# Performance work log

Hardware: AMD Instinct MI355X
Metric: run time of the kernel (lower is better)

## Reference

```python
import math
import jax, jax.numpy as jnp
import numpy as np

BS, N, NH_N, NH_E, NH_Y, H = 2, 256, 256, 128, 128, 8
F = NH_N // H  # per-head feature dim


def _lin(x, w, b):
    # w stored as (in, out): out = x @ w + b
    return x @ w + b


def setup_inputs() -> dict:
    key = jax.random.key(0)
    ks = iter(jax.random.split(key, 64))
    def w(shape, s=0.02):
        return jax.random.normal(next(ks), shape, dtype=jnp.float32) * s
    inp = {
        'x': jax.random.normal(next(ks), (BS, N, NH_N), dtype=jnp.float32),
        'a': jax.random.normal(next(ks), (BS, N, N, NH_E), dtype=jnp.float32),
        'y': jax.random.normal(next(ks), (BS, NH_Y), dtype=jnp.float32),
        'qw': w((NH_N, NH_N)), 'qb': w((NH_N,)),
        'kw': w((NH_N, NH_N)), 'kb': w((NH_N,)),
        'vw': w((NH_N, NH_N)), 'vb': w((NH_N,)),
        'a2x_add_w': w((NH_E, NH_N)), 'a2x_add_b': w((NH_N,)),
        'a2x_mul_w': w((NH_E, NH_N)), 'a2x_mul_b': w((NH_N,)),
        'y2e_mul_w': w((NH_Y, NH_N)), 'y2e_mul_b': w((NH_N,)),
        'y2e_add_w': w((NH_Y, NH_N)), 'y2e_add_b': w((NH_N,)),
        'y2x_mul_w': w((NH_Y, NH_N)), 'y2x_mul_b': w((NH_N,)),
        'y2x_add_w': w((NH_Y, NH_N)), 'y2x_add_b': w((NH_N,)),
        'y_y_w': w((NH_Y, NH_Y)), 'y_y_b': w((NH_Y,)),
        'x_y_w': w((4 * NH_N, NH_Y)), 'x_y_b': w((NH_Y,)),
        'a_y_w': w((4 * NH_E, NH_Y)), 'a_y_b': w((NH_Y,)),
        'x_out_w': w((NH_N, NH_N)), 'x_out_b': w((NH_N,)),
        'a_out_w': w((NH_N, NH_E)), 'a_out_b': w((NH_E,)),
        'y_out1_w': w((NH_Y, NH_Y)), 'y_out1_b': w((NH_Y,)),
        'y_out2_w': w((NH_Y, NH_Y)), 'y_out2_b': w((NH_Y,)),
    }
    return inp


def reference(x, a, y, qw, qb, kw, kb, vw, vb,
              a2x_add_w, a2x_add_b, a2x_mul_w, a2x_mul_b,
              y2e_mul_w, y2e_mul_b, y2e_add_w, y2e_add_b,
              y2x_mul_w, y2x_mul_b, y2x_add_w, y2x_add_b,
              y_y_w, y_y_b, x_y_w, x_y_b, a_y_w, a_y_b,
              x_out_w, x_out_b, a_out_w, a_out_b,
              y_out1_w, y_out1_b, y_out2_w, y_out2_b):
    bs, n, _ = x.shape
    Q = _lin(x, qw, qb).reshape(bs, n, H, F)
    K = _lin(x, kw, kb).reshape(bs, n, H, F)
    # Feature-wise outer product (never reduced over F): (bs, n, n, H, F)
    Y = (Q[:, :, None] * K[:, None, :]) / math.sqrt(F)
    a1 = _lin(a, a2x_add_w, a2x_add_b).reshape(bs, n, n, H, F)
    a2 = _lin(a, a2x_mul_w, a2x_mul_b).reshape(bs, n, n, H, F)
    Y = Y * (a1 + 1.0) + a2
    # edge output path
    ahat = Y.reshape(bs, n, n, NH_N)
    ye1 = _lin(y, y2e_add_w, y2e_add_b)[:, None, None]
    ye2 = _lin(y, y2e_mul_w, y2e_mul_b)[:, None, None]
    ahat = _lin(ye1 + (ye2 + 1.0) * ahat, a_out_w, a_out_b)
    # node output path: softmax over the second node axis (dim=2)
    attn = jax.nn.softmax(Y, axis=2)
    V = _lin(x, vw, vb).reshape(bs, n, H, F)
    wV = jnp.einsum('bijhf,bjhf->bihf', attn, V).reshape(bs, n, NH_N)
    yx1 = _lin(y, y2x_add_w, y2x_add_b)[:, None]
    yx2 = _lin(y, y2x_mul_w, y2x_mul_b)[:, None]
    xhat = _lin(yx1 + (yx2 + 1.0) * wV, x_out_w, x_out_b)
    # global output path (Xtoy / Atoy use unbiased std, ddof=1 as in torch.std)
    zx = jnp.concatenate([x.mean(axis=1), x.min(axis=1), x.max(axis=1),
                          jnp.std(x, axis=1, ddof=1)], axis=-1)
    za = jnp.concatenate([a.mean(axis=(1, 2)), a.min(axis=(1, 2)), a.max(axis=(1, 2)),
                          jnp.std(a, axis=(1, 2), ddof=1)], axis=-1)
    yhat = _lin(y, y_y_w, y_y_b) + _lin(za, a_y_w, a_y_b) + _lin(zx, x_y_w, x_y_b)
    yhat = _lin(jax.nn.relu(_lin(yhat, y_out1_w, y_out1_b)), y_out2_w, y_out2_b)
    return (xhat, ahat, yhat)
```

## Files before the change

kernel.cpp:

```cpp
#include <hip/hip_runtime.h>
#include <hip/hip_bf16.h>
#include <cstddef>

constexpr int BS = 2;
constexpr int N  = 256;
constexpr int D  = 256;
constexpr int E  = 128;
constexpr int YD = 128;
constexpr float RSQRT_F = 0.17677669529663687f;

typedef __attribute__((ext_vector_type(8))) short     short8;
typedef __attribute__((ext_vector_type(4))) float     f32x4;
typedef __attribute__((ext_vector_type(4))) unsigned short u16x4;
typedef __attribute__((ext_vector_type(8))) unsigned short u16x8;

__device__ __forceinline__ unsigned short f2bf(float x) {
    unsigned u = __float_as_uint(x);
    unsigned r = (u + 0x7fffu + ((u >> 16) & 1u)) >> 16;
    return (unsigned short)r;
}
__device__ __forceinline__ float bf2f(unsigned short h) {
    return __uint_as_float(((unsigned)h) << 16);
}
__device__ __forceinline__ f32x4 mfma16(short8 a, short8 b, f32x4 c) {
    return __builtin_amdgcn_mfma_f32_16x16x32_bf16(a, b, c, 0, 0, 0);
}

__global__ __launch_bounds__(256) void prep_kernel(
        const float* __restrict__ x, const float* __restrict__ a,
        const float* __restrict__ y,
        const float* __restrict__ qw, const float* __restrict__ qb,
        const float* __restrict__ kw, const float* __restrict__ kb,
        const float* __restrict__ vw, const float* __restrict__ vb,
        const float* __restrict__ Wadd, const float* __restrict__ Wmul,
        const float* __restrict__ W2,
        const float* __restrict__ we_add, const float* __restrict__ be_add,
        const float* __restrict__ we_mul, const float* __restrict__ be_mul,
        const float* __restrict__ wx_add, const float* __restrict__ bx_add,
        const float* __restrict__ wx_mul, const float* __restrict__ bx_mul,
        float* __restrict__ Q, unsigned short* __restrict__ kvJ,
        unsigned short* __restrict__ WaddT, unsigned short* __restrict__ WmulT,
        unsigned short* __restrict__ W2T,
        float* __restrict__ ye1, float* __restrict__ ye2,
        float* __restrict__ yx1, float* __restrict__ yx2,
        float* __restrict__ psum, float* __restrict__ psumsq,
        float* __restrict__ pmin, float* __restrict__ pmax,
        float* __restrict__ zx) {
    const int blk = blockIdx.x;
    const int tid = threadIdx.x;
    __shared__ float smem[4096];

    if (blk < 192) {
        const int m  = blk >> 6;
        const int rg = blk & 63;
        const float* W = (m == 0) ? qw : (m == 1) ? kw : vw;
        const float* B = (m == 0) ? qb : (m == 1) ? kb : vb;
        float (*xs)[D] = (float(*)[D])smem;
#pragma unroll
        for (int r = 0; r < 8; ++r)
            xs[r][tid] = x[(size_t)(rg * 8 + r) * D + tid];
        __syncthreads();
        float acc[8];
        const float bb = B[tid];
#pragma unroll
        for (int r = 0; r < 8; ++r) acc[r] = bb;
#pragma unroll 4
        for (int k = 0; k < D; ++k) {
            const float w = W[k * D + tid];
#pragma unroll
            for (int r = 0; r < 8; ++r) acc[r] += xs[r][k] * w;
        }
#pragma unroll
        for (int r = 0; r < 8; ++r) {
            const int row = rg * 8 + r;
            if (m == 0) Q[(size_t)row * D + tid] = acc[r];
            else        kvJ[((size_t)row * D + tid) * 2 + (m - 1)] = f2bf(acc[r]);
        }
    } else if (blk < 576) {
        int idx = (blk - 192) * 256 + tid;
        int s = idx >> 15;
        int k = idx & 32767;
        if (s == 0)      { int f = k >> 7, e = k & 127; WaddT[k] = f2bf(Wadd[e * 256 + f]); }
        else if (s == 1) { int f = k >> 7, e = k & 127; WmulT[k] = f2bf(Wmul[e * 256 + f]); }
        else             { int f = k & 255, e = k >> 8; W2T[k]   = f2bf(W2[f * 128 + e]); }
    } else if (blk < 584) {
        const int bb = (blk - 576) >> 2;
        const int m  = (blk - 576) & 3;
        const float* W; const float* B; float* O;
        switch (m) {
            case 0:  W = we_add; B = be_add; O = ye1; break;
            case 1:  W = we_mul; B = be_mul; O = ye2; break;
            case 2:  W = wx_add; B = bx_add; O = yx1; break;
            default: W = wx_mul; B = bx_mul; O = yx2; break;
        }
        float acc = B[tid];
#pragma unroll 4
        for (int k = 0; k < YD; ++k)
            acc += y[bb * YD + k] * W[k * D + tid];
        O[bb * D + tid] = acc;
    } else if (blk < 600) {
        const int bb = (blk - 584) >> 3;
        const int fc = (blk - 584) & 7;
        const int fl = tid & 31;
        const int ig = tid >> 5;
        const int f  = fc * 32 + fl;
        float s = 0.f, ss = 0.f, mn = INFINITY, mx = -INFINITY;
#pragma unroll 4
        for (int i = ig * 32; i < ig * 32 + 32; ++i) {
            const float v = x[((size_t)bb * N + i) * D + f];
            s += v; ss += v * v; mn = fminf(mn, v); mx = fmaxf(mx, v);
        }
        smem[0 * 256 + ig * 32 + fl] = s;
        smem[1 * 256 + ig * 32 + fl] = ss;
        smem[2 * 256 + ig * 32 + fl] = mn;
        smem[3 * 256 + ig * 32 + fl] = mx;
        __syncthreads();
        if (ig == 0) {
#pragma unroll
            for (int gg = 1; gg < 8; ++gg) {
                s += smem[0 * 256 + gg * 32 + fl]; ss += smem[1 * 256 + gg * 32 + fl];
                mn = fminf(mn, smem[2 * 256 + gg * 32 + fl]);
                mx = fmaxf(mx, smem[3 * 256 + gg * 32 + fl]);
            }
            const float M = 256.f;
            const float mean = s / M;
            const float var  = (ss - s * s / M) / (M - 1.f);
            zx[bb * 1024 + f]       = mean;
            zx[bb * 1024 + 256 + f] = mn;
            zx[bb * 1024 + 512 + f] = mx;
            zx[bb * 1024 + 768 + f] = sqrtf(fmaxf(var, 0.f));
        }
    } else {
        const int bi2 = blk - 600;
        const int te  = tid & 31;
        const int tj  = tid >> 5;
        const float* base = a + (size_t)bi2 * N * E + te * 4;
        f32x4 s4  = (f32x4){0.f, 0.f, 0.f, 0.f};
        f32x4 ss4 = (f32x4){0.f, 0.f, 0.f, 0.f};
        f32x4 mn4 = (f32x4){INFINITY, INFINITY, INFINITY, INFINITY};
        f32x4 mx4 = (f32x4){-INFINITY, -INFINITY, -INFINITY, -INFINITY};
#pragma unroll 4
        for (int j = tj * 32; j < tj * 32 + 32; ++j) {
            const f32x4 v = *(const f32x4*)(base + (size_t)j * E);
            s4 += v;
            ss4.x = fmaf(v.x, v.x, ss4.x); ss4.y = fmaf(v.y, v.y, ss4.y);
            ss4.z = fmaf(v.z, v.z, ss4.z); ss4.w = fmaf(v.w, v.w, ss4.w);
            mn4.x = fminf(mn4.x, v.x); mn4.y = fminf(mn4.y, v.y);
            mn4.z = fminf(mn4.z, v.z); mn4.w = fminf(mn4.w, v.w);
            mx4.x = fmaxf(mx4.x, v.x); mx4.y = fmaxf(mx4.y, v.y);
            mx4.z = fmaxf(mx4.z, v.z); mx4.w = fmaxf(mx4.w, v.w);
        }
        *(f32x4*)(smem + (0 * 8 + tj) * 128 + te * 4) = s4;
        *(f32x4*)(smem + (1 * 8 + tj) * 128 + te * 4) = ss4;
        *(f32x4*)(smem + (2 * 8 + tj) * 128 + te * 4) = mn4;
        *(f32x4*)(smem + (3 * 8 + tj) * 128 + te * 4) = mx4;
        __syncthreads();
        if (tid < 128) {
            float s = 0.f, ss = 0.f, mn = INFINITY, mx = -INFINITY;
#pragma unroll
            for (int g = 0; g < 8; ++g) {
                s  += smem[(0 * 8 + g) * 128 + tid];
                ss += smem[(1 * 8 + g) * 128 + tid];
                mn = fminf(mn, smem[(2 * 8 + g) * 128 + tid]);
                mx = fmaxf(mx, smem[(3 * 8 + g) * 128 + tid]);
            }
            const int o = bi2 * E + tid;
            psum[o] = s; psumsq[o] = ss; pmin[o] = mn; pmax[o] = mx;
        }
    }
}

__global__ __launch_bounds__(512, 1) void main_kernel(
        const float* __restrict__ a,
        const unsigned short* __restrict__ WaddT, const float* __restrict__ Badd,
        const unsigned short* __restrict__ WmulT, const float* __restrict__ Bmul,
        const unsigned short* __restrict__ W2T,  const float* __restrict__ AoutB,
        const float* __restrict__ Q, const unsigned short* __restrict__ kvJ,
        const float* __restrict__ ye1, const float* __restrict__ ye2,
        float* __restrict__ ahat, float* __restrict__ wV) {
    const int bi = ((blockIdx.x & 7) << 6) | (blockIdx.x >> 3);
    const int b  = bi >> 8;
    const int tid  = threadIdx.x;
    const int lane = tid & 63;
    const int w    = tid >> 6;
    const int l15  = lane & 15;
    const int lk   = lane >> 4;

    __shared__ unsigned short abuf[2][32 * 128];
    __shared__ unsigned short hbuf[2][32 * 256];

    const float* arow = a + (size_t)bi * (N * E);
    float* ahatp      = ahat + (size_t)bi * (N * E);
    const unsigned short* kvb = kvJ + (size_t)b * N * D * 2;

    short8 waf[4][2], wmf[4][2], w2f[8];
#pragma unroll
    for (int ks = 0; ks < 4; ++ks)
#pragma unroll
        for (int m_ = 0; m_ < 2; ++m_) {
            const int frow = w * 32 + m_ * 16 + l15;
            waf[ks][m_] = *(const short8*)(WaddT + frow * 128 + ks * 32 + lk * 8);
            wmf[ks][m_] = *(const short8*)(WmulT + frow * 128 + ks * 32 + lk * 8);
        }
#pragma unroll
    for (int ks = 0; ks < 8; ++ks)
        w2f[ks] = *(const short8*)(W2T + (w * 16 + l15) * 256 + ks * 32 + lk * 8);

    float qs[8], e1c[8], e2c[8], b1c[8], b2c[8];
#pragma unroll
    for (int m_ = 0; m_ < 2; ++m_) {
        const int f0 = w * 32 + m_ * 16 + lk * 4;
        const f32x4 qv = *(const f32x4*)(Q + (size_t)bi * D + f0);
        const f32x4 a1 = *(const f32x4*)(ye1 + b * D + f0);
        const f32x4 a2 = *(const f32x4*)(ye2 + b * D + f0);
        const f32x4 bb1 = *(const f32x4*)(Badd + f0);
        const f32x4 bb2 = *(const f32x4*)(Bmul + f0);
#pragma unroll
        for (int r = 0; r < 4; ++r) {
            const int fi = m_ * 4 + r;
            qs[fi]  = qv[r] * RSQRT_F;
            e1c[fi] = a1[r];
            e2c[fi] = a2[r] + 1.f;
            b1c[fi] = bb1[r] + 1.f;
            b2c[fi] = bb2[r];
        }
    }
    const f32x4 bias2 = *(const f32x4*)(AoutB + w * 16 + lk * 4);

    float sm_l[8], sm_a[8];
#pragma unroll
    for (int q = 0; q < 8; ++q) { sm_l[q] = 0.f; sm_a[q] = 0.f; }

    const int sjl = tid >> 4;
    const int seq = tid & 15;
    const unsigned saddr = ((unsigned)(sjl * 256 + seq * 16)) ^ ((unsigned)(sjl & 7) << 4);

    {
        const float* ap = arow + (size_t)sjl * E + seq * 8;
        const f32x4 v0 = *(const f32x4*)ap;
        const f32x4 v1 = *(const f32x4*)(ap + 4);
        u16x8 pk;
        pk.s0 = f2bf(v0.x); pk.s1 = f2bf(v0.y); pk.s2 = f2bf(v0.z); pk.s3 = f2bf(v0.w);
        pk.s4 = f2bf(v1.x); pk.s5 = f2bf(v1.y); pk.s6 = f2bf(v1.z); pk.s7 = f2bf(v1.w);
        *(u16x8*)((char*)abuf[0] + saddr) = pk;
    }
    __syncthreads();

    for (int t = 0; t < 8; ++t) {
        const int j0 = t * 32;
        const unsigned short* ab = abuf[t & 1];
        unsigned short* hw = hbuf[t & 1];

        f32x4 p0, p1;
        if (t < 7) {
            const float* ap = arow + (size_t)(j0 + 32 + sjl) * E + seq * 8;
            p0 = *(const f32x4*)ap;
            p1 = *(const f32x4*)(ap + 4);
        }
        u16x8 kvv[2][2];
#pragma unroll
        for (int n_ = 0; n_ < 2; ++n_) {
            const int jg = j0 + n_ * 16 + l15;
#pragma unroll
            for (int m_ = 0; m_ < 2; ++m_)
                kvv[n_][m_] = *(const u16x8*)(kvb + ((size_t)jg * D + w * 32 + m_ * 16 + lk * 4) * 2);
        }

        f32x4 acc1[2][2], acc2[2][2];
#pragma unroll
        for (int m_ = 0; m_ < 2; ++m_) {
            const f32x4 i1 = (f32x4){b1c[m_ * 4 + 0], b1c[m_ * 4 + 1], b1c[m_ * 4 + 2], b1c[m_ * 4 + 3]};
            const f32x4 i2 = (f32x4){b2c[m_ * 4 + 0], b2c[m_ * 4 + 1], b2c[m_ * 4 + 2], b2c[m_ * 4 + 3]};
#pragma unroll
            for (int n_ = 0; n_ < 2; ++n_) { acc1[m_][n_] = i1; acc2[m_][n_] = i2; }
        }
#pragma unroll
        for (int ks = 0; ks < 4; ++ks) {
            short8 bfrg[2];
#pragma unroll
            for (int n_ = 0; n_ < 2; ++n_) {
                const int jrow = n_ * 16 + l15;
                const unsigned baddr = ((unsigned)(jrow * 256 + (ks * 32 + lk * 8) * 2))
                                       ^ ((unsigned)(jrow & 7) << 4);
                bfrg[n_] = *(const short8*)((const char*)ab + baddr);
            }
#pragma unroll
            for (int m_ = 0; m_ < 2; ++m_)
#pragma unroll
                for (int n_ = 0; n_ < 2; ++n_) {
                    acc1[m_][n_] = mfma16(waf[ks][m_], bfrg[n_], acc1[m_][n_]);
                    acc2[m_][n_] = mfma16(wmf[ks][m_], bfrg[n_], acc2[m_][n_]);
                }
        }

#pragma unroll
        for (int n_ = 0; n_ < 2; ++n_) {
            const int jrow = n_ * 16 + l15;
#pragma unroll
            for (int m_ = 0; m_ < 2; ++m_) {
                u16x4 hp;
#pragma unroll
                for (int r = 0; r < 4; ++r) {
                    const int fi = m_ * 4 + r;
                    const float kf = bf2f(kvv[n_][m_][2 * r]);
                    const float vf = bf2f(kvv[n_][m_][2 * r + 1]);
                    const float yv = qs[fi] * kf * acc1[m_][n_][r] + acc2[m_][n_][r];
                    hp[r] = f2bf(e1c[fi] + e2c[fi] * yv);
                    const float ev = __expf(yv);
                    sm_l[fi] += ev;
                    sm_a[fi] += ev * vf;
                }
                const unsigned haddr = ((unsigned)(jrow * 512 + (w * 32 + m_ * 16 + lk * 4) * 2))
                                       ^ ((unsigned)(jrow & 7) << 4);
                *(u16x4*)((char*)hw + haddr) = hp;
            }
        }

        if (t < 7) {
            u16x8 pk;
            pk.s0 = f2bf(p0.x); pk.s1 = f2bf(p0.y); pk.s2 = f2bf(p0.z); pk.s3 = f2bf(p0.w);
            pk.s4 = f2bf(p1.x); pk.s5 = f2bf(p1.y); pk.s6 = f2bf(p1.z); pk.s7 = f2bf(p1.w);
            *(u16x8*)((char*)abuf[(t + 1) & 1] + saddr) = pk;
        }
        __syncthreads();

        f32x4 accO[2];
        accO[0] = bias2; accO[1] = bias2;
#pragma unroll
        for (int ks = 0; ks < 8; ++ks) {
            const int foff = ks * 32 + lk * 8;
#pragma unroll
            for (int n2 = 0; n2 < 2; ++n2) {
                const int jrow = n2 * 16 + l15;
                const unsigned haddr = ((unsigned)(jrow * 512 + foff * 2))
                                       ^ ((unsigned)(jrow & 7) << 4);
                const short8 hf = *(const short8*)((const char*)hw + haddr);
                accO[n2] = mfma16(w2f[ks], hf, accO[n2]);
            }
        }
        {
            const int eb = w * 16 + lk * 4;
#pragma unroll
            for (int n2 = 0; n2 < 2; ++n2) {
                const int jg2 = j0 + n2 * 16 + l15;
                *(f32x4*)(ahatp + (size_t)jg2 * E + eb) = accO[n2];
            }
        }
    }

#pragma unroll
    for (int st = 1; st <= 8; st <<= 1) {
#pragma unroll
        for (int fi = 0; fi < 8; ++fi) {
            sm_l[fi] += __shfl_xor(sm_l[fi], st, 64);
            sm_a[fi] += __shfl_xor(sm_a[fi], st, 64);
        }
    }
    if (l15 == 0) {
#pragma unroll
        for (int m_ = 0; m_ < 2; ++m_)
#pragma unroll
            for (int r = 0; r < 4; ++r) {
                const int fi = m_ * 4 + r;
                const int f  = w * 32 + m_ * 16 + lk * 4 + r;
                wV[(size_t)bi * D + f] = sm_a[fi] / sm_l[fi];
            }
    }
}

__global__ __launch_bounds__(256) void post_kernel(
        const float* __restrict__ wV,
        const float* __restrict__ yx1, const float* __restrict__ yx2,
        const float* __restrict__ W, const float* __restrict__ B,
        const float* __restrict__ psum, const float* __restrict__ psumsq,
        const float* __restrict__ pmin, const float* __restrict__ pmax,
        float* __restrict__ xhat, float* __restrict__ za) {
    const int blk = blockIdx.x;
    const int tid = threadIdx.x;
    __shared__ float smem[2048];

    if (blk < 64) {
        float (*xr)[D] = (float(*)[D])smem;
#pragma unroll
        for (int r = 0; r < 8; ++r) {
            const int row = blk * 8 + r;
            const int b = row >> 8;
            xr[r][tid] = yx1[b * D + tid] + (yx2[b * D + tid] + 1.f) * wV[(size_t)row * D + tid];
        }
        __syncthreads();
        float acc[8];
        const float bb = B[tid];
#pragma unroll
        for (int r = 0; r < 8; ++r) acc[r] = bb;
#pragma unroll 4
        for (int k = 0; k < D; ++k) {
            const float w = W[k * D + tid];
#pragma unroll
            for (int r = 0; r < 8; ++r) acc[r] += xr[r][k] * w;
        }
#pragma unroll
        for (int r = 0; r < 8; ++r)
            xhat[(size_t)(blk * 8 + r) * D + tid] = acc[r];
    } else {
        const int b = blk - 64;
        const int feat = tid & 127;
        const int g = tid >> 7;
        float s = 0.f, ss = 0.f, mn = INFINITY, mx = -INFINITY;
#pragma unroll 4
        for (int c = g * 128; c < g * 128 + 128; ++c) {
            const int o = (b * 256 + c) * E + feat;
            s += psum[o]; ss += psumsq[o];
            mn = fminf(mn, pmin[o]); mx = fmaxf(mx, pmax[o]);
        }
        smem[0 * 256 + g * 128 + feat] = s;
        smem[1 * 256 + g * 128 + feat] = ss;
        smem[2 * 256 + g * 128 + feat] = mn;
        smem[3 * 256 + g * 128 + feat] = mx;
        __syncthreads();
        if (g == 0) {
            s += smem[0 * 256 + 128 + feat]; ss += smem[1 * 256 + 128 + feat];
            mn = fminf(mn, smem[2 * 256 + 128 + feat]);
            mx = fmaxf(mx, smem[3 * 256 + 128 + feat]);
            const float M = 65536.f;
            const float mean = s / M;
            const float var  = (ss - s * s / M) / (M - 1.f);
            za[b * 512 + feat]       = mean;
            za[b * 512 + 128 + feat] = mn;
            za[b * 512 + 256 + feat] = mx;
            za[b * 512 + 384 + feat] = sqrtf(fmaxf(var, 0.f));
        }
    }
}

__global__ __launch_bounds__(128) void yhat_partial_kernel(
        const float* __restrict__ y,
        const float* __restrict__ za, const float* __restrict__ zx,
        const float* __restrict__ yyw, const float* __restrict__ ayw,
        const float* __restrict__ xyw,
        float* __restrict__ partial) {
    const int b = blockIdx.x >> 6 ? 1 : 0;
    const int bb = blockIdx.x / 52;
    const int c  = blockIdx.x - bb * 52;
    const int o  = threadIdx.x;
    const int k0 = c * 32;
    float p = 0.f;
    if (k0 < 128) {
#pragma unroll 8
        for (int k = k0; k < k0 + 32; ++k) p += y[bb * YD + k] * yyw[k * YD + o];
    } else if (k0 < 640) {
        const int kk = k0 - 128;
#pragma unroll 8
        for (int k = kk; k < kk + 32; ++k) p += za[bb * 512 + k] * ayw[k * YD + o];
    } else {
        const int kk = k0 - 640;
#pragma unroll 8
        for (int k = kk; k < kk + 32; ++k) p += zx[bb * 1024 + k] * xyw[k * YD + o];
    }
    (void)b;
    partial[(bb * 52 + c) * YD + o] = p;
}

__global__ __launch_bounds__(512) void yhat_finish_kernel(
        const float* __restrict__ partial,
        const float* __restrict__ yyb, const float* __restrict__ xyb,
        const float* __restrict__ ayb,
        const float* __restrict__ w1, const float* __restrict__ b1,
        const float* __restrict__ w2, const float* __restrict__ b2,
        float* __restrict__ out) {
    const int b = blockIdx.x;
    const int tid = threadIdx.x;
    const int o = tid & 127;
    const int q = tid >> 7;
    __shared__ float red[4][128];
    __shared__ float h1s[128], h2s[128];
    float s = 0.f;
#pragma unroll 13
    for (int c = q * 13; c < q * 13 + 13; ++c)
        s += partial[(b * 52 + c) * YD + o];
    red[q][o] = s;
    __syncthreads();
    if (tid < 128)
        h1s[o] = yyb[o] + xyb[o] + ayb[o] + red[0][o] + red[1][o] + red[2][o] + red[3][o];
    __syncthreads();
    float p2 = 0.f;
#pragma unroll 8
    for (int k = q * 32; k < q * 32 + 32; ++k) p2 += h1s[k] * w1[k * YD + o];
    red[q][o] = p2;
    __syncthreads();
    if (tid < 128) h2s[o] = fmaxf(b1[o] + red[0][o] + red[1][o] + red[2][o] + red[3][o], 0.f);
    __syncthreads();
    float p3 = 0.f;
#pragma unroll 8
    for (int k = q * 32; k < q * 32 + 32; ++k) p3 += h2s[k] * w2[k * YD + o];
    red[q][o] = p3;
    __syncthreads();
    if (tid < 128) out[b * YD + o] = b2[o] + red[0][o] + red[1][o] + red[2][o] + red[3][o];
}

extern "C" void kernel_launch(void* const* d_in, const int* in_sizes, int n_in,
                              void* d_out, int out_size, void* d_ws, size_t ws_size,
                              hipStream_t stream) {
    const float* x         = (const float*)d_in[0];
    const float* a         = (const float*)d_in[1];
    const float* y         = (const float*)d_in[2];
    const float* qw        = (const float*)d_in[3];  const float* qb        = (const float*)d_in[4];
    const float* kw        = (const float*)d_in[5];  const float* kb        = (const float*)d_in[6];
    const float* vw        = (const float*)d_in[7];  const float* vb        = (const float*)d_in[8];
    const float* a2x_add_w = (const float*)d_in[9];  const float* a2x_add_b = (const float*)d_in[10];
    const float* a2x_mul_w = (const float*)d_in[11]; const float* a2x_mul_b = (const float*)d_in[12];
    const float* y2e_mul_w = (const float*)d_in[13]; const float* y2e_mul_b = (const float*)d_in[14];
    const float* y2e_add_w = (const float*)d_in[15]; const float* y2e_add_b = (const float*)d_in[16];
    const float* y2x_mul_w = (const float*)d_in[17]; const float* y2x_mul_b = (const float*)d_in[18];
    const float* y2x_add_w = (const float*)d_in[19]; const float* y2x_add_b = (const float*)d_in[20];
    const float* y_y_w     = (const float*)d_in[21]; const float* y_y_b     = (const float*)d_in[22];
    const float* x_y_w     = (const float*)d_in[23]; const float* x_y_b     = (const float*)d_in[24];
    const float* a_y_w     = (const float*)d_in[25]; const float* a_y_b     = (const float*)d_in[26];
    const float* x_out_w   = (const float*)d_in[27]; const float* x_out_b   = (const float*)d_in[28];
    const float* a_out_w   = (const float*)d_in[29]; const float* a_out_b   = (const float*)d_in[30];
    const float* y_out1_w  = (const float*)d_in[31]; const float* y_out1_b  = (const float*)d_in[32];
    const float* y_out2_w  = (const float*)d_in[33]; const float* y_out2_b  = (const float*)d_in[34];

    float* ws = (float*)d_ws;
    float* Q      = ws;
    unsigned short* kvJ = (unsigned short*)(ws + 131072);
    float* wV     = ws + 262144;
    float* ye1    = ws + 393216;
    float* ye2    = ws + 393728;
    float* yx1    = ws + 394240;
    float* yx2    = ws + 394752;
    float* psum   = ws + 395264;
    float* psumsq = ws + 460800;
    float* pminb  = ws + 526336;
    float* pmaxb  = ws + 591872;
    float* za     = ws + 657408;
    float* zx     = ws + 658432;
    unsigned short* WaddT = (unsigned short*)(ws + 660480);
    unsigned short* WmulT = (unsigned short*)(ws + 676864);
    unsigned short* W2T   = (unsigned short*)(ws + 693248);
    float* ypart  = ws + 709632;

    float* xhat = (float*)d_out;
    float* ahat = (float*)d_out + 131072;
    float* yhat = (float*)d_out + 16908288;

    prep_kernel<<<1112, 256, 0, stream>>>(
        x, a, y, qw, qb, kw, kb, vw, vb,
        a2x_add_w, a2x_mul_w, a_out_w,
        y2e_add_w, y2e_add_b, y2e_mul_w, y2e_mul_b,
        y2x_add_w, y2x_add_b, y2x_mul_w, y2x_mul_b,
        Q, kvJ, WaddT, WmulT, W2T,
        ye1, ye2, yx1, yx2,
        psum, psumsq, pminb, pmaxb, zx);
    main_kernel<<<512, 512, 0, stream>>>(a, WaddT, a2x_add_b, WmulT, a2x_mul_b,
                                         W2T, a_out_b, Q, kvJ, ye1, ye2, ahat, wV);
    post_kernel<<<66, 256, 0, stream>>>(wV, yx1, yx2, x_out_w, x_out_b,
                                        psum, psumsq, pminb, pmaxb, xhat, za);
    yhat_partial_kernel<<<104, 128, 0, stream>>>(y, za, zx, y_y_w, a_y_w, x_y_w, ypart);
    yhat_finish_kernel<<<2, 512, 0, stream>>>(ypart, y_y_b, x_y_b, a_y_b,
                                              y_out1_w, y_out1_b, y_out2_w, y_out2_b, yhat);
}
```

Before: 115.8 us.

## Double j-tile to 64 rows per iteration in main kernel, halving barriers

The main kernel now processes 64 edge rows per pipeline step instead of 32, with doubled LDS buffers. That halves the loop iterations and __syncthreads count and issues four prefetch loads per thread with a new staging layout. It also switches bf16 conversion to the HIP intrinsic, raises one unroll factor, and drops the occupancy hint from launch bounds. The cost is doubled shared memory (about 96KB) and more live registers, which may limit occupancy or cause spills.

```diff
diff --git a/kernel.cpp b/kernel.cpp
--- a/kernel.cpp
+++ b/kernel.cpp
@@ -1,6 +1,7 @@
 #include <hip/hip_runtime.h>
 #include <hip/hip_bf16.h>
 #include <cstddef>
+#include <cstring>
 
 constexpr int BS = 2;
 constexpr int N  = 256;
@@ -15,9 +16,10 @@
 typedef __attribute__((ext_vector_type(8))) unsigned short u16x8;
 
 __device__ __forceinline__ unsigned short f2bf(float x) {
-    unsigned u = __float_as_uint(x);
-    unsigned r = (u + 0x7fffu + ((u >> 16) & 1u)) >> 16;
-    return (unsigned short)r;
+    __hip_bfloat16 h = __float2bfloat16(x);
+    unsigned short r;
+    __builtin_memcpy(&r, &h, 2);
+    return r;
 }
 __device__ __forceinline__ float bf2f(unsigned short h) {
     return __uint_as_float(((unsigned)h) << 16);
@@ -139,7 +141,7 @@
         f32x4 ss4 = (f32x4){0.f, 0.f, 0.f, 0.f};
         f32x4 mn4 = (f32x4){INFINITY, INFINITY, INFINITY, INFINITY};
         f32x4 mx4 = (f32x4){-INFINITY, -INFINITY, -INFINITY, -INFINITY};
-#pragma unroll 4
+#pragma unroll 8
         for (int j = tj * 32; j < tj * 32 + 32; ++j) {
             const f32x4 v = *(const f32x4*)(base + (size_t)j * E);
             s4 += v;
@@ -170,7 +172,7 @@
     }
 }
 
-__global__ __launch_bounds__(512, 1) void main_kernel(
+__global__ __launch_bounds__(512) void main_kernel(
         const float* __restrict__ a,
         const unsigned short* __restrict__ WaddT, const float* __restrict__ Badd,
         const unsigned short* __restrict__ WmulT, const float* __restrict__ Bmul,
@@ -186,8 +188,8 @@
     const int l15  = lane & 15;
     const int lk   = lane >> 4;
 
-    __shared__ unsigned short abuf[2][32 * 128];
-    __shared__ unsigned short hbuf[2][32 * 256];
+    __shared__ unsigned short abuf[2][64 * 128];
+    __shared__ unsigned short hbuf[2][64 * 256];
 
     const float* arow = a + (size_t)bi * (N * E);
     float* ahatp      = ahat + (size_t)bi * (N * E);
@@ -210,9 +212,9 @@
 #pragma unroll
     for (int m_ = 0; m_ < 2; ++m_) {
         const int f0 = w * 32 + m_ * 16 + lk * 4;
-        const f32x4 qv = *(const f32x4*)(Q + (size_t)bi * D + f0);
-        const f32x4 a1 = *(const f32x4*)(ye1 + b * D + f0);
-        const f32x4 a2 = *(const f32x4*)(ye2 + b * D + f0);
+        const f32x4 qv  = *(const f32x4*)(Q + (size_t)bi * D + f0);
+        const f32x4 a1  = *(const f32x4*)(ye1 + b * D + f0);
+        const f32x4 a2  = *(const f32x4*)(ye2 + b * D + f0);
         const f32x4 bb1 = *(const f32x4*)(Badd + f0);
         const f32x4 bb2 = *(const f32x4*)(Bmul + f0);
 #pragma unroll
@@ -231,109 +233,123 @@
 #pragma unroll
     for (int q = 0; q < 8; ++q) { sm_l[q] = 0.f; sm_a[q] = 0.f; }
 
-    const int sjl = tid >> 4;
-    const int seq = tid & 15;
-    const unsigned saddr = ((unsigned)(sjl * 256 + seq * 16)) ^ ((unsigned)(sjl & 7) << 4);
+    const int echunk = tid & 31;
+    const int rowgrp = tid >> 5;
 
     {
-        const float* ap = arow + (size_t)sjl * E + seq * 8;
-        const f32x4 v0 = *(const f32x4*)ap;
-        const f32x4 v1 = *(const f32x4*)(ap + 4);
-        u16x8 pk;
-        pk.s0 = f2bf(v0.x); pk.s1 = f2bf(v0.y); pk.s2 = f2bf(v0.z); pk.s3 = f2bf(v0.w);
-        pk.s4 = f2bf(v1.x); pk.s5 = f2bf(v1.y); pk.s6 = f2bf(v1.z); pk.s7 = f2bf(v1.w);
-        *(u16x8*)((char*)abuf[0] + saddr) = pk;
+        const float* ap = arow + (size_t)(rowgrp * 4) * E + echunk * 4;
+#pragma unroll
+        for (int rr = 0; rr < 4; ++rr) {
+            const f32x4 v = *(const f32x4*)(ap + (size_t)rr * E);
+            u16x4 pk;
+            pk.x = f2bf(v.x); pk.y = f2bf(v.y); pk.z = f2bf(v.z); pk.w = f2bf(v.w);
+            const int row = rowgrp * 4 + rr;
+            const unsigned addr = ((unsigned)(row * 256 + echunk * 8)) ^ ((unsigned)(row & 7) << 4);
+            *(u16x4*)((char*)abuf[0] + addr) = pk;
+        }
     }
     __syncthreads();
 
-    for (int t = 0; t < 8; ++t) {
-        const int j0 = t * 32;
+    for (int t = 0; t < 4; ++t) {
+        const int j0 = t * 64;
         const unsigned short* ab = abuf[t & 1];
         unsigned short* hw = hbuf[t & 1];
 
-        f32x4 p0, p1;
-        if (t < 7) {
-            const float* ap = arow + (size_t)(j0 + 32 + sjl) * E + seq * 8;
-            p0 = *(const f32x4*)ap;
-            p1 = *(const f32x4*)(ap + 4);
-        }
-        u16x8 kvv[2][2];
-#pragma unroll
-        for (int n_ = 0; n_ < 2; ++n_) {
-            const int jg = j0 + n_ * 16 + l15;
-#pragma unroll
-            for (int m_ = 0; m_ < 2; ++m_)
-                kvv[n_][m_] = *(const u16x8*)(kvb + ((size_t)jg * D + w * 32 + m_ * 16 + lk * 4) * 2);
-        }
-
-        f32x4 acc1[2][2], acc2[2][2];
-#pragma unroll
-        for (int m_ = 0; m_ < 2; ++m_) {
-            const f32x4 i1 = (f32x4){b1c[m_ * 4 + 0], b1c[m_ * 4 + 1], b1c[m_ * 4 + 2], b1c[m_ * 4 + 3]};
-            const f32x4 i2 = (f32x4){b2c[m_ * 4 + 0], b2c[m_ * 4 + 1], b2c[m_ * 4 + 2], b2c[m_ * 4 + 3]};
-#pragma unroll
-            for (int n_ = 0; n_ < 2; ++n_) { acc1[m_][n_] = i1; acc2[m_][n_] = i2; }
-        }
-#pragma unroll
-        for (int ks = 0; ks < 4; ++ks) {
-            short8 bfrg[2];
+        f32x4 p0, p1, p2, p3;
+        if (t < 3) {
+            const float* ap = arow + (size_t)(j0 + 64 + rowgrp * 4) * E + echunk * 4;
+            p0 = *(const f32x4*)(ap);
+            p1 = *(const f32x4*)(ap + E);
+            p2 = *(const f32x4*)(ap + 2 * E);
+            p3 = *(const f32x4*)(ap + 3 * E);
+        }
+
+#pragma unroll
+        for (int h2 = 0; h2 < 2; ++h2) {
+            u16x8 kvv[2][2];
 #pragma unroll
             for (int n_ = 0; n_ < 2; ++n_) {
-                const int jrow = n_ * 16 + l15;
-                const unsigned baddr = ((unsigned)(jrow * 256 + (ks * 32 + lk * 8) * 2))
-                                       ^ ((unsigned)(jrow & 7) << 4);
-                bfrg[n_] = *(const short8*)((const char*)ab + baddr);
-            }
-#pragma unroll
-            for (int m_ = 0; m_ < 2; ++m_)
+                const int jg = j0 + h2 * 32 + n_ * 16 + l15;
+#pragma unroll
+                for (int m_ = 0; m_ < 2; ++m_)
+                    kvv[n_][m_] = *(const u16x8*)(kvb + ((size_t)jg * D + w * 32 + m_ * 16 + lk * 4) * 2);
+            }
+            f32x4 acc1[2][2], acc2[2][2];
+#pragma unroll
+            for (int m_ = 0; m_ < 2; ++m_) {
+                const f32x4 i1 = (f32x4){b1c[m_ * 4 + 0], b1c[m_ * 4 + 1], b1c[m_ * 4 + 2], b1c[m_ * 4 + 3]};
+                const f32x4 i2 = (f32x4){b2c[m_ * 4 + 0], b2c[m_ * 4 + 1], b2c[m_ * 4 + 2], b2c[m_ * 4 + 3]};
+#pragma unroll
+                for (int n_ = 0; n_ < 2; ++n_) { acc1[m_][n_] = i1; acc2[m_][n_] = i2; }
+            }
+#pragma unroll
+            for (int ks = 0; ks < 4; ++ks) {
+                short8 bfrg[2];
 #pragma unroll
                 for (int n_ = 0; n_ < 2; ++n_) {
-                    acc1[m_][n_] = mfma16(waf[ks][m_], bfrg[n_], acc1[m_][n_]);
-                    acc2[m_][n_] = mfma16(wmf[ks][m_], bfrg[n_], acc2[m_][n_]);
+                    const int jloc = h2 * 32 + n_ * 16 + l15;
+                    const unsigned baddr = ((unsigned)(jloc * 256 + (ks * 32 + lk * 8) * 2))
+                                           ^ ((unsigned)(jloc & 7) << 4);
+                    bfrg[n_] = *(const short8*)((const char*)ab + baddr);
                 }
-        }
-
-#pragma unroll
-        for (int n_ = 0; n_ < 2; ++n_) {
-            const int jrow = n_ * 16 + l15;
-#pragma unroll
-            for (int m_ = 0; m_ < 2; ++m_) {
-                u16x4 hp;
-#pragma unroll
-                for (int r = 0; r < 4; ++r) {
-                    const int fi = m_ * 4 + r;
-                    const float kf = bf2f(kvv[n_][m_][2 * r]);
-                    const float vf = bf2f(kvv[n_][m_][2 * r + 1]);
-                    const float yv = qs[fi] * kf * acc1[m_][n_][r] + acc2[m_][n_][r];
-                    hp[r] = f2bf(e1c[fi] + e2c[fi] * yv);
-                    const float ev = __expf(yv);
-                    sm_l[fi] += ev;
-                    sm_a[fi] += ev * vf;
+#pragma unroll
+                for (int m_ = 0; m_ < 2; ++m_)
+#pragma unroll
+                    for (int n_ = 0; n_ < 2; ++n_) {
+                        acc1[m_][n_] = mfma16(waf[ks][m_], bfrg[n_], acc1[m_][n_]);
+                        acc2[m_][n_] = mfma16(wmf[ks][m_], bfrg[n_], acc2[m_][n_]);
+                    }
+            }
+#pragma unroll
+            for (int n_ = 0; n_ < 2; ++n_) {
+                const int jloc = h2 * 32 + n_ * 16 + l15;
+#pragma unroll
+                for (int m_ = 0; m_ < 2; ++m_) {
+                    u16x4 hp;
+#pragma unroll
+                    for (int r = 0; r < 4; ++r) {
+                        const int fi = m_ * 4 + r;
+                        const float kf = bf2f(kvv[n_][m_][2 * r]);
+                        const float vf = bf2f(kvv[n_][m_][2 * r + 1]);
+                        const float yv = qs[fi] * kf * acc1[m_][n_][r] + acc2[m_][n_][r];
+                        hp[r] = f2bf(e1c[fi] + e2c[fi] * yv);
+                        const float ev = __expf(yv);
+                        sm_l[fi] += ev;
+                        sm_a[fi] += ev * vf;
+                    }
+                    const unsigned haddr = ((unsigned)(jloc * 512 + (w * 32 + m_ * 16 + lk * 4) * 2))
+                                           ^ ((unsigned)(jloc & 7) << 4);
+                    *(u16x4*)((char*)hw + haddr) = hp;
                 }
-                const unsigned haddr = ((unsigned)(jrow * 512 + (w * 32 + m_ * 16 + lk * 4) * 2))
-                                       ^ ((unsigned)(jrow & 7) << 4);
-                *(u16x4*)((char*)hw + haddr) = hp;
-            }
-        }
-
-        if (t < 7) {
-            u16x8 pk;
-            pk.s0 = f2bf(p0.x); pk.s1 = f2bf(p0.y); pk.s2 = f2bf(p0.z); pk.s3 = f2bf(p0.w);
-            pk.s4 = f2bf(p1.x); pk.s5 = f2bf(p1.y); pk.s6 = f2bf(p1.z); pk.s7 = f2bf(p1.w);
-            *(u16x8*)((char*)abuf[(t + 1) & 1] + saddr) = pk;
+            }
+        }
+
+        if (t < 3) {
+            unsigned short* nb = abuf[(t + 1) & 1];
+            const f32x4 pv[4] = {p0, p1, p2, p3};
+#pragma unroll
+            for (int rr = 0; rr < 4; ++rr) {
+                u16x4 pk;
+                pk.x = f2bf(pv[rr].x); pk.y = f2bf(pv[rr].y);
+                pk.z = f2bf(pv[rr].z); pk.w = f2bf(pv[rr].w);
+                const int row = rowgrp * 4 + rr;
+                const unsigned addr = ((unsigned)(row * 256 + echunk * 8)) ^ ((unsigned)(row & 7) << 4);
+                *(u16x4*)((char*)nb + addr) = pk;
+            }
         }
         __syncthreads();
 
-        f32x4 accO[2];
-        accO[0] = bias2; accO[1] = bias2;
+        f32x4 accO[4];
+#pragma unroll
+        for (int n2 = 0; n2 < 4; ++n2) accO[n2] = bias2;
 #pragma unroll
         for (int ks = 0; ks < 8; ++ks) {
             const int foff = ks * 32 + lk * 8;
 #pragma unroll
-            for (int n2 = 0; n2 < 2; ++n2) {
-                const int jrow = n2 * 16 + l15;
-                const unsigned haddr = ((unsigned)(jrow * 512 + foff * 2))
-                                       ^ ((unsigned)(jrow & 7) << 4);
+            for (int n2 = 0; n2 < 4; ++n2) {
+                const int jloc = n2 * 16 + l15;
+                const unsigned haddr = ((unsigned)(jloc * 512 + foff * 2))
+                                       ^ ((unsigned)(jloc & 7) << 4);
                 const short8 hf = *(const short8*)((const char*)hw + haddr);
                 accO[n2] = mfma16(w2f[ks], hf, accO[n2]);
             }
@@ -341,7 +357,7 @@
         {
             const int eb = w * 16 + lk * 4;
 #pragma unroll
-            for (int n2 = 0; n2 < 2; ++n2) {
+            for (int n2 = 0; n2 < 4; ++n2) {
                 const int jg2 = j0 + n2 * 16 + l15;
                 *(f32x4*)(ahatp + (size_t)jg2 * E + eb) = accO[n2];
             }
@@ -438,7 +454,6 @@
         const float* __restrict__ yyw, const float* __restrict__ ayw,
         const float* __restrict__ xyw,
         float* __restrict__ partial) {
-    const int b = blockIdx.x >> 6 ? 1 : 0;
     const int bb = blockIdx.x / 52;
     const int c  = blockIdx.x - bb * 52;
     const int o  = threadIdx.x;
@@ -456,7 +471,6 @@
 #pragma unroll 8
         for (int k = kk; k < kk + 32; ++k) p += zx[bb * 1024 + k] * xyw[k * YD + o];
     }
-    (void)b;
     partial[(bb * 52 + c) * YD + o] = p;
 }
 
```

After: 216.8 us. 1.87x slower.

## Fuse edge-tensor statistics into main kernel's tile loading pass

Applied to the files above, without the earlier changes.

The per-row mean/min/max/sumsq statistics over the edge tensor move out of prep_kernel and into main_kernel, computed on the fp32 values already loaded for bf16 staging. This removes a second full read of the 64 MB edge tensor and 512 prep blocks. The staging layout changes to 2 rows by 4 elements per thread. W2 fragments are now reloaded from global memory each iteration instead of held in registers, which cuts register pressure but adds repeated loads. A reduction through shared memory is added at the end of main_kernel.

```diff
diff --git a/kernel.cpp b/kernel.cpp
--- a/kernel.cpp
+++ b/kernel.cpp
@@ -1,6 +1,7 @@
 #include <hip/hip_runtime.h>
 #include <hip/hip_bf16.h>
 #include <cstddef>
+#include <cstring>
 
 constexpr int BS = 2;
 constexpr int N  = 256;
@@ -27,7 +28,7 @@
 }
 
 __global__ __launch_bounds__(256) void prep_kernel(
-        const float* __restrict__ x, const float* __restrict__ a,
+        const float* __restrict__ x,
         const float* __restrict__ y,
         const float* __restrict__ qw, const float* __restrict__ qb,
         const float* __restrict__ kw, const float* __restrict__ kb,
@@ -43,12 +44,10 @@
         unsigned short* __restrict__ W2T,
         float* __restrict__ ye1, float* __restrict__ ye2,
         float* __restrict__ yx1, float* __restrict__ yx2,
-        float* __restrict__ psum, float* __restrict__ psumsq,
-        float* __restrict__ pmin, float* __restrict__ pmax,
         float* __restrict__ zx) {
     const int blk = blockIdx.x;
     const int tid = threadIdx.x;
-    __shared__ float smem[4096];
+    __shared__ float smem[2048];
 
     if (blk < 192) {
         const int m  = blk >> 6;
@@ -98,7 +97,7 @@
         for (int k = 0; k < YD; ++k)
             acc += y[bb * YD + k] * W[k * D + tid];
         O[bb * D + tid] = acc;
-    } else if (blk < 600) {
+    } else {
         const int bb = (blk - 584) >> 3;
         const int fc = (blk - 584) & 7;
         const int fl = tid & 31;
@@ -130,43 +129,6 @@
             zx[bb * 1024 + 512 + f] = mx;
             zx[bb * 1024 + 768 + f] = sqrtf(fmaxf(var, 0.f));
         }
-    } else {
-        const int bi2 = blk - 600;
-        const int te  = tid & 31;
-        const int tj  = tid >> 5;
-        const float* base = a + (size_t)bi2 * N * E + te * 4;
-        f32x4 s4  = (f32x4){0.f, 0.f, 0.f, 0.f};
-        f32x4 ss4 = (f32x4){0.f, 0.f, 0.f, 0.f};
-        f32x4 mn4 = (f32x4){INFINITY, INFINITY, INFINITY, INFINITY};
-        f32x4 mx4 = (f32x4){-INFINITY, -INFINITY, -INFINITY, -INFINITY};
-#pragma unroll 4
-        for (int j = tj * 32; j < tj * 32 + 32; ++j) {
-            const f32x4 v = *(const f32x4*)(base + (size_t)j * E);
-            s4 += v;
-            ss4.x = fmaf(v.x, v.x, ss4.x); ss4.y = fmaf(v.y, v.y, ss4.y);
-            ss4.z = fmaf(v.z, v.z, ss4.z); ss4.w = fmaf(v.w, v.w, ss4.w);
-            mn4.x = fminf(mn4.x, v.x); mn4.y = fminf(mn4.y, v.y);
-            mn4.z = fminf(mn4.z, v.z); mn4.w = fminf(mn4.w, v.w);
-            mx4.x = fmaxf(mx4.x, v.x); mx4.y = fmaxf(mx4.y, v.y);
-            mx4.z = fmaxf(mx4.z, v.z); mx4.w = fmaxf(mx4.w, v.w);
-        }
-        *(f32x4*)(smem + (0 * 8 + tj) * 128 + te * 4) = s4;
-        *(f32x4*)(smem + (1 * 8 + tj) * 128 + te * 4) = ss4;
-        *(f32x4*)(smem + (2 * 8 + tj) * 128 + te * 4) = mn4;
-        *(f32x4*)(smem + (3 * 8 + tj) * 128 + te * 4) = mx4;
-        __syncthreads();
-        if (tid < 128) {
-            float s = 0.f, ss = 0.f, mn = INFINITY, mx = -INFINITY;
-#pragma unroll
-            for (int g = 0; g < 8; ++g) {
-                s  += smem[(0 * 8 + g) * 128 + tid];
-                ss += smem[(1 * 8 + g) * 128 + tid];
-                mn = fminf(mn, smem[(2 * 8 + g) * 128 + tid]);
-                mx = fmaxf(mx, smem[(3 * 8 + g) * 128 + tid]);
-            }
-            const int o = bi2 * E + tid;
-            psum[o] = s; psumsq[o] = ss; pmin[o] = mn; pmax[o] = mx;
-        }
     }
 }
 
@@ -177,7 +139,9 @@
         const unsigned short* __restrict__ W2T,  const float* __restrict__ AoutB,
         const float* __restrict__ Q, const unsigned short* __restrict__ kvJ,
         const float* __restrict__ ye1, const float* __restrict__ ye2,
-        float* __restrict__ ahat, float* __restrict__ wV) {
+        float* __restrict__ ahat, float* __restrict__ wV,
+        float* __restrict__ psum, float* __restrict__ psumsq,
+        float* __restrict__ pmin, float* __restrict__ pmax) {
     const int bi = ((blockIdx.x & 7) << 6) | (blockIdx.x >> 3);
     const int b  = bi >> 8;
     const int tid  = threadIdx.x;
@@ -193,7 +157,7 @@
     float* ahatp      = ahat + (size_t)bi * (N * E);
     const unsigned short* kvb = kvJ + (size_t)b * N * D * 2;
 
-    short8 waf[4][2], wmf[4][2], w2f[8];
+    short8 waf[4][2], wmf[4][2];
 #pragma unroll
     for (int ks = 0; ks < 4; ++ks)
 #pragma unroll
@@ -202,9 +166,6 @@
             waf[ks][m_] = *(const short8*)(WaddT + frow * 128 + ks * 32 + lk * 8);
             wmf[ks][m_] = *(const short8*)(WmulT + frow * 128 + ks * 32 + lk * 8);
         }
-#pragma unroll
-    for (int ks = 0; ks < 8; ++ks)
-        w2f[ks] = *(const short8*)(W2T + (w * 16 + l15) * 256 + ks * 32 + lk * 8);
 
     float qs[8], e1c[8], e2c[8], b1c[8], b2c[8];
 #pragma unroll
@@ -231,18 +192,34 @@
 #pragma unroll
     for (int q = 0; q < 8; ++q) { sm_l[q] = 0.f; sm_a[q] = 0.f; }
 
-    const int sjl = tid >> 4;
-    const int seq = tid & 15;
-    const unsigned saddr = ((unsigned)(sjl * 256 + seq * 16)) ^ ((unsigned)(sjl & 7) << 4);
+    f32x4 st_s  = (f32x4){0.f, 0.f, 0.f, 0.f};
+    f32x4 st_ss = (f32x4){0.f, 0.f, 0.f, 0.f};
+    f32x4 st_mn = (f32x4){INFINITY, INFINITY, INFINITY, INFINITY};
+    f32x4 st_mx = (f32x4){-INFINITY, -INFINITY, -INFINITY, -INFINITY};
+
+#define STAT4(v) { st_s += (v); \
+                   st_ss.x = fmaf((v).x,(v).x,st_ss.x); st_ss.y = fmaf((v).y,(v).y,st_ss.y); \
+                   st_ss.z = fmaf((v).z,(v).z,st_ss.z); st_ss.w = fmaf((v).w,(v).w,st_ss.w); \
+                   st_mn.x = fminf(st_mn.x,(v).x); st_mn.y = fminf(st_mn.y,(v).y); \
+                   st_mn.z = fminf(st_mn.z,(v).z); st_mn.w = fminf(st_mn.w,(v).w); \
+                   st_mx.x = fmaxf(st_mx.x,(v).x); st_mx.y = fmaxf(st_mx.y,(v).y); \
+                   st_mx.z = fmaxf(st_mx.z,(v).z); st_mx.w = fmaxf(st_mx.w,(v).w); }
+
+    const int echunk = tid & 31;
+    const int rowgrp = tid >> 5;
 
     {
-        const float* ap = arow + (size_t)sjl * E + seq * 8;
-        const f32x4 v0 = *(const f32x4*)ap;
-        const f32x4 v1 = *(const f32x4*)(ap + 4);
-        u16x8 pk;
-        pk.s0 = f2bf(v0.x); pk.s1 = f2bf(v0.y); pk.s2 = f2bf(v0.z); pk.s3 = f2bf(v0.w);
-        pk.s4 = f2bf(v1.x); pk.s5 = f2bf(v1.y); pk.s6 = f2bf(v1.z); pk.s7 = f2bf(v1.w);
-        *(u16x8*)((char*)abuf[0] + saddr) = pk;
+        const float* ap = arow + (size_t)(rowgrp * 2) * E + echunk * 4;
+#pragma unroll
+        for (int rr = 0; rr < 2; ++rr) {
+            const f32x4 v = *(const f32x4*)(ap + (size_t)rr * E);
+            STAT4(v);
+            u16x4 pk;
+            pk.x = f2bf(v.x); pk.y = f2bf(v.y); pk.z = f2bf(v.z); pk.w = f2bf(v.w);
+            const int row = rowgrp * 2 + rr;
+            const unsigned addr = ((unsigned)(row * 256 + echunk * 8)) ^ ((unsigned)(row & 7) << 4);
+            *(u16x4*)((char*)abuf[0] + addr) = pk;
+        }
     }
     __syncthreads();
 
@@ -253,9 +230,9 @@
 
         f32x4 p0, p1;
         if (t < 7) {
-            const float* ap = arow + (size_t)(j0 + 32 + sjl) * E + seq * 8;
+            const float* ap = arow + (size_t)(j0 + 32 + rowgrp * 2) * E + echunk * 4;
             p0 = *(const f32x4*)ap;
-            p1 = *(const f32x4*)(ap + 4);
+            p1 = *(const f32x4*)(ap + E);
         }
         u16x8 kvv[2][2];
 #pragma unroll
@@ -317,13 +294,25 @@
         }
 
         if (t < 7) {
-            u16x8 pk;
-            pk.s0 = f2bf(p0.x); pk.s1 = f2bf(p0.y); pk.s2 = f2bf(p0.z); pk.s3 = f2bf(p0.w);
-            pk.s4 = f2bf(p1.x); pk.s5 = f2bf(p1.y); pk.s6 = f2bf(p1.z); pk.s7 = f2bf(p1.w);
-            *(u16x8*)((char*)abuf[(t + 1) & 1] + saddr) = pk;
+            STAT4(p0); STAT4(p1);
+            unsigned short* nb = abuf[(t + 1) & 1];
+            const f32x4 pv[2] = {p0, p1};
+#pragma unroll
+            for (int rr = 0; rr < 2; ++rr) {
+                u16x4 pk;
+                pk.x = f2bf(pv[rr].x); pk.y = f2bf(pv[rr].y);
+                pk.z = f2bf(pv[rr].z); pk.w = f2bf(pv[rr].w);
+                const int row = rowgrp * 2 + rr;
+                const unsigned addr = ((unsigned)(row * 256 + echunk * 8)) ^ ((unsigned)(row & 7) << 4);
+                *(u16x4*)((char*)nb + addr) = pk;
+            }
         }
         __syncthreads();
 
+        short8 w2v[8];
+#pragma unroll
+        for (int ks = 0; ks < 8; ++ks)
+            w2v[ks] = *(const short8*)(W2T + (w * 16 + l15) * 256 + ks * 32 + lk * 8);
         f32x4 accO[2];
         accO[0] = bias2; accO[1] = bias2;
 #pragma unroll
@@ -335,7 +324,7 @@
                 const unsigned haddr = ((unsigned)(jrow * 512 + foff * 2))
                                        ^ ((unsigned)(jrow & 7) << 4);
                 const short8 hf = *(const short8*)((const char*)hw + haddr);
-                accO[n2] = mfma16(w2f[ks], hf, accO[n2]);
+                accO[n2] = mfma16(w2v[ks], hf, accO[n2]);
             }
         }
         {
@@ -366,6 +355,30 @@
                 wV[(size_t)bi * D + f] = sm_a[fi] / sm_l[fi];
             }
     }
+
+    __syncthreads();
+    {
+        float* sc = (float*)hbuf;
+        const int ebase = echunk * 4;
+        *(f32x4*)(sc + (0 * 16 + rowgrp) * 128 + ebase) = st_s;
+        *(f32x4*)(sc + (1 * 16 + rowgrp) * 128 + ebase) = st_ss;
+        *(f32x4*)(sc + (2 * 16 + rowgrp) * 128 + ebase) = st_mn;
+        *(f32x4*)(sc + (3 * 16 + rowgrp) * 128 + ebase) = st_mx;
+        __syncthreads();
+        if (tid < 128) {
+            float s = 0.f, ss = 0.f, mn = INFINITY, mx = -INFINITY;
+#pragma unroll
+            for (int g = 0; g < 16; ++g) {
+                s  += sc[(0 * 16 + g) * 128 + tid];
+                ss += sc[(1 * 16 + g) * 128 + tid];
+                mn = fminf(mn, sc[(2 * 16 + g) * 128 + tid]);
+                mx = fmaxf(mx, sc[(3 * 16 + g) * 128 + tid]);
+            }
+            const int o = bi * E + tid;
+            psum[o] = s; psumsq[o] = ss; pmin[o] = mn; pmax[o] = mx;
+        }
+    }
+#undef STAT4
 }
 
 __global__ __launch_bounds__(256) void post_kernel(
@@ -438,7 +451,6 @@
         const float* __restrict__ yyw, const float* __restrict__ ayw,
         const float* __restrict__ xyw,
         float* __restrict__ partial) {
-    const int b = blockIdx.x >> 6 ? 1 : 0;
     const int bb = blockIdx.x / 52;
     const int c  = blockIdx.x - bb * 52;
     const int o  = threadIdx.x;
@@ -456,7 +468,6 @@
 #pragma unroll 8
         for (int k = kk; k < kk + 32; ++k) p += zx[bb * 1024 + k] * xyw[k * YD + o];
     }
-    (void)b;
     partial[(bb * 52 + c) * YD + o] = p;
 }
 
@@ -543,16 +554,16 @@
     float* ahat = (float*)d_out + 131072;
     float* yhat = (float*)d_out + 16908288;
 
-    prep_kernel<<<1112, 256, 0, stream>>>(
-        x, a, y, qw, qb, kw, kb, vw, vb,
+    prep_kernel<<<600, 256, 0, stream>>>(
+        x, y, qw, qb, kw, kb, vw, vb,
         a2x_add_w, a2x_mul_w, a_out_w,
         y2e_add_w, y2e_add_b, y2e_mul_w, y2e_mul_b,
         y2x_add_w, y2x_add_b, y2x_mul_w, y2x_mul_b,
         Q, kvJ, WaddT, WmulT, W2T,
-        ye1, ye2, yx1, yx2,
-        psum, psumsq, pminb, pmaxb, zx);
+        ye1, ye2, yx1, yx2, zx);
     main_kernel<<<512, 512, 0, stream>>>(a, WaddT, a2x_add_b, WmulT, a2x_mul_b,
-                                         W2T, a_out_b, Q, kvJ, ye1, ye2, ahat, wV);
+                                         W2T, a_out_b, Q, kvJ, ye1, ye2, ahat, wV,
+                                         psum, psumsq, pminb, pmaxb);
     post_kernel<<<66, 256, 0, stream>>>(wV, yx1, yx2, x_out_w, x_out_b,
                                         psum, psumsq, pminb, pmaxb, xhat, za);
     yhat_partial_kernel<<<104, 128, 0, stream>>>(y, za, zx, y_y_w, a_y_w, x_y_w, ypart);
```

Result: slower. 122.8 us (+6.0%).
